# Kernel optimization log

Measured on AMD Instinct MI355X. Metric: run time of the kernel, lower is better.

## Reference

```python
import jax, jax.numpy as jnp
import numpy as np

VOXEL_SIZE = (0.075, 0.075, 0.2)
PC_MIN = (-54.0, -54.0, -5.0)
GRID = (1440, 1440, 40)      # (gx, gy, gz) = round((pc_max - pc_min) / voxel_size)
MAX_PTS = 10                 # max points per voxel
MAX_VOX = 160000             # max voxels (train)


def setup_inputs() -> dict:
    key = jax.random.key(0)
    N, C = 2_000_000, 5
    u = jax.random.uniform(key, (N, C), dtype=jnp.float32)
    lo = jnp.array([-54.0, -54.0, -5.0, 0.0, 0.0], jnp.float32)
    span = jnp.array([108.0, 108.0, 8.0, 1.0, 1.0], jnp.float32)
    return {"points": u * span + lo}


def reference(points):
    # Faithful PointToVoxel semantics: bin points into voxels, voxels ordered by
    # first point occurrence (hash-table insertion order), cap points-per-voxel
    # and voxel count, return (voxels, coords_zyx, num_points_per_voxel).
    N, C = points.shape
    gx, gy, gz = GRID
    vsize = jnp.array(VOXEL_SIZE, jnp.float32)
    pmin = jnp.array(PC_MIN, jnp.float32)

    c = jnp.floor((points[:, :3] - pmin) / vsize).astype(jnp.int32)  # [N,3] xyz voxel coords
    valid = jnp.all((c >= 0) & (c < jnp.array([gx, gy, gz], jnp.int32)), axis=1)
    lin = (c[:, 2].astype(jnp.int64) * gy + c[:, 1]) * gx + c[:, 0]  # z-major linear id
    sent = jnp.int64(gx) * gy * gz                                    # sentinel for invalid
    lin = jnp.where(valid, lin, sent)

    # Sort by (voxel id, point index): groups points by voxel, earliest point first.
    order = jnp.argsort(lin * N + jnp.arange(N, dtype=jnp.int64))
    slin = lin[order]
    valid_s = slin < sent
    new = jnp.concatenate([valid_s[:1], (slin[1:] != slin[:-1]) & valid_s[1:]])
    gid = jnp.maximum(jnp.cumsum(new.astype(jnp.int32)) - 1, 0)       # group id per sorted point

    # First (smallest) original point index per voxel group -> insertion order rank.
    first_idx = jnp.full((N,), N, jnp.int32).at[gid].min(
        jnp.where(valid_s, order, N).astype(jnp.int32), mode="drop")
    ranks = jnp.argsort(jnp.argsort(first_idx)).astype(jnp.int32)     # voxel insertion rank

    # Slot of each point within its voxel group.
    idx32 = jnp.arange(N, dtype=jnp.int32)
    starts = jax.lax.associative_scan(jnp.maximum, jnp.where(new, idx32, 0))
    pos = idx32 - starts

    r = ranks[gid]
    keep = valid_s & (r < MAX_VOX) & (pos < MAX_PTS)
    vox_idx = jnp.where(keep, r, MAX_VOX)   # MAX_VOX = out-of-bounds -> dropped
    slot = jnp.where(keep, pos, 0)

    voxels = jnp.zeros((MAX_VOX, MAX_PTS, C), points.dtype).at[vox_idx, slot].set(
        points[order], mode="drop")
    num_points = jnp.zeros((MAX_VOX,), jnp.int32).at[vox_idx].add(1, mode="drop")
    czyx = c[:, ::-1][order]                # spconv returns coords as (z, y, x)
    coords = jnp.zeros((MAX_VOX, 3), jnp.int32).at[vox_idx].set(czyx, mode="drop")
    return voxels, coords, num_points
```

## Files before the change

### kernel.cpp

```cpp
#include <hip/hip_runtime.h>

#define GX 1440
#define GY 1440
#define GZ 40
#define MAX_PTS 10
#define MAX_VOX 160000
#define NC 40
#define CAPC 65536
#define CHUNK 4096
#define L2CHUNKS (CAPC / CHUNK)
#define NFINE 10240
#define CAPB2 512
#define PA_BLOCKS 1024
#define PA_ITERS 8
#define GSTRIDE 16
#define EMPTY32 0xFFFFFFFFu
#define EMPTY64 0xFFFFFFFFFFFFFFFFull
#define BCAP (1 << 19)
#define NBLKB (BCAP / 256)
#define TAILB ((MAX_VOX + 255) / 256)
#define HG 65536
#define MCAP 12
#define ST_PARTIAL (1ull << 62)
#define ST_PREFIX  (2ull << 62)
#define ST_VAL     ((1ull << 62) - 1)

__global__ void pa1_scatter(const float* __restrict__ pts, int n,
                            unsigned long long* __restrict__ pairs1,
                            int* __restrict__ gcur1) {
    __shared__ int hist[NC];
    if (threadIdx.x < NC) hist[threadIdx.x] = 0;
    __syncthreads();
    int per = (n + PA_BLOCKS - 1) / PA_BLOCKS;
    int i0 = blockIdx.x * per;
    int i1 = i0 + per; if (i1 > n) i1 = n;
    int lin[PA_ITERS];
#pragma unroll
    for (int u = 0; u < PA_ITERS; ++u) {
        int i = i0 + u * 256 + (int)threadIdx.x;
        int l = -1;
        if (i < i1) {
            float x = pts[i * 5 + 0];
            float y = pts[i * 5 + 1];
            float z = pts[i * 5 + 2];
            int cx = (int)floorf((x - (-54.0f)) / 0.075f);
            int cy = (int)floorf((y - (-54.0f)) / 0.075f);
            int cz = (int)floorf((z - (-5.0f)) / 0.2f);
            if (cx >= 0 && cx < GX && cy >= 0 && cy < GY && cz >= 0 && cz < GZ)
                l = (cz * GY + cy) * GX + cx;
        }
        lin[u] = l;
        if (l >= 0) atomicAdd(&hist[l >> 21], 1);
    }
    __syncthreads();
    if (threadIdx.x < NC) {
        int h = hist[threadIdx.x];
        hist[threadIdx.x] =
            (h > 0) ? atomicAdd(&gcur1[threadIdx.x * GSTRIDE], h) : 0;
    }
    __syncthreads();
#pragma unroll
    for (int u = 0; u < PA_ITERS; ++u) {
        int l = lin[u];
        if (l < 0) continue;
        int i = i0 + u * 256 + (int)threadIdx.x;
        int c = l >> 21;
        int pos = atomicAdd(&hist[c], 1);
        if (pos < CAPC)
            pairs1[(size_t)c * CAPC + pos] =
                ((unsigned long long)(unsigned)l << 32) | (unsigned)i;
    }
}

__global__ void pa2_scatter(const unsigned long long* __restrict__ pairs1,
                            const int* __restrict__ gcur1,
                            unsigned long long* __restrict__ pairs2,
                            int* __restrict__ gcur2) {
    __shared__ int cur[256];
    int c = blockIdx.x >> 4;
    int j = blockIdx.x & (L2CHUNKS - 1);
    cur[threadIdx.x] = 0;
    __syncthreads();
    int cnt = gcur1[c * GSTRIDE]; if (cnt > CAPC) cnt = CAPC;
    int t0 = j * CHUNK;
    int t1 = t0 + CHUNK; if (t1 > cnt) t1 = cnt;
    const unsigned long long* bp = pairs1 + (size_t)c * CAPC;
    unsigned long long pr[CHUNK / 256];
#pragma unroll
    for (int u = 0; u < CHUNK / 256; ++u) {
        int t = t0 + u * 256 + (int)threadIdx.x;
        pr[u] = (t < t1) ? bp[t] : EMPTY64;
        if (pr[u] != EMPTY64)
            atomicAdd(&cur[(unsigned)(pr[u] >> 45) & 255u], 1);
    }
    __syncthreads();
    {
        int h = cur[threadIdx.x];
        cur[threadIdx.x] =
            (h > 0)
                ? atomicAdd(&gcur2[((c << 8) + threadIdx.x) * GSTRIDE], h)
                : 0;
    }
    __syncthreads();
#pragma unroll
    for (int u = 0; u < CHUNK / 256; ++u) {
        if (pr[u] == EMPTY64) continue;
        int f = (int)((unsigned)(pr[u] >> 45) & 255u);
        int pos = atomicAdd(&cur[f], 1);
        if (pos < CAPB2)
            pairs2[(size_t)((c << 8) + f) * CAPB2 + pos] = pr[u];
    }
}

__global__ void pb_build(const unsigned long long* __restrict__ pairs2,
                         const int* __restrict__ gcur2,
                         unsigned char* __restrict__ marks8,
                         unsigned int* __restrict__ hkey,
                         unsigned int* __restrict__ hcnt,
                         unsigned int* __restrict__ hmem) {
    __shared__ unsigned int mn[8192];
    __shared__ unsigned int multibit[256];
    int fid = blockIdx.x;
    int n = gcur2[fid * GSTRIDE]; if (n > CAPB2) n = CAPB2;
    uint4* mn4 = (uint4*)mn;
    uint4 e4 = make_uint4(EMPTY32, EMPTY32, EMPTY32, EMPTY32);
#pragma unroll
    for (int u = 0; u < 8; ++u) mn4[u * 256 + threadIdx.x] = e4;
    multibit[threadIdx.x] = 0;
    __syncthreads();
    const unsigned long long* bp = pairs2 + (size_t)fid * CAPB2;
    unsigned int lcell[CAPB2 / 256];
    unsigned int lidx[CAPB2 / 256];
#pragma unroll
    for (int u = 0; u < CAPB2 / 256; ++u) {
        int t = u * 256 + (int)threadIdx.x;
        unsigned cell = EMPTY32, idx = 0;
        if (t < n) {
            unsigned long long pr = bp[t];
            cell = ((unsigned)(pr >> 32)) & 8191u;
            idx = (unsigned)pr;
        }
        lcell[u] = cell;
        lidx[u] = idx;
        if (cell != EMPTY32) atomicMin(&mn[cell], idx);
    }
    __syncthreads();
#pragma unroll
    for (int u = 0; u < CAPB2 / 256; ++u) {
        unsigned cell = lcell[u];
        if (cell == EMPTY32) continue;
        unsigned m = mn[cell];
        if (m != lidx[u]) {
            atomicOr(&multibit[cell >> 5], 1u << (cell & 31));
            if (m < BCAP) {
                unsigned key = m + 1u;
                unsigned h = (m * 2654435761u) >> 16;
                while (true) {
                    unsigned prev = atomicCAS(&hkey[h], 0u, key);
                    if (prev == 0u || prev == key) break;
                    h = (h + 1) & (HG - 1);
                }
                unsigned pos = atomicAdd(&hcnt[h], 1u);
                if (pos < MCAP) hmem[h * MCAP + pos] = lidx[u];
            }
        }
    }
    __syncthreads();
#pragma unroll
    for (int u = 0; u < CAPB2 / 256; ++u) {
        unsigned cell = lcell[u];
        if (cell != EMPTY32 && mn[cell] == lidx[u] && lidx[u] < BCAP)
            marks8[lidx[u]] = (unsigned char)(
                1u + ((multibit[cell >> 5] >> (cell & 31)) & 1u));
    }
}

__global__ void pfx_fill(const float* __restrict__ pts,
                         const unsigned char* __restrict__ marks8,
                         unsigned long long* __restrict__ dstate,
                         const unsigned int* __restrict__ hkey,
                         const unsigned int* __restrict__ hcnt,
                         const unsigned int* __restrict__ hmem,
                         float* __restrict__ vox, float* __restrict__ coords,
                         float* __restrict__ nump) {
    int t = blockIdx.x;
    int tid = threadIdx.x, lane = tid & 63, wv = tid >> 6;
    if (t >= NBLKB) {
        int r = (t - NBLKB) * 256 + tid;
        if (r >= MAX_VOX) return;
        unsigned long long s = 0;
        if (lane == 0)
            do { s = atomicAdd(&dstate[NBLKB - 1], 0ull); } while ((s >> 62) != 2);
        int V = (int)__shfl((int)(s & ST_VAL), 0, 64);
        if (V > MAX_VOX) V = MAX_VOX;
        if (r < V) return;
        float* row = vox + (size_t)r * (MAX_PTS * 5);
        for (int k = 0; k < MAX_PTS * 5; ++k) row[k] = 0.0f;
        coords[r * 3 + 0] = 0.0f;
        coords[r * 3 + 1] = 0.0f;
        coords[r * 3 + 2] = 0.0f;
        nump[r] = 0.0f;
        return;
    }
    __shared__ unsigned cw[4];
    __shared__ int sh_prefix;
    int i = t * 256 + tid;
    int m8 = marks8[i];
    unsigned long long b = __ballot(m8 != 0);
    if (lane == 0) cw[wv] = (unsigned)__popcll(b);
    __syncthreads();
    int c = (int)(cw[0] + cw[1] + cw[2] + cw[3]);
    if (tid == 0) atomicExch(&dstate[t], ST_PARTIAL | (unsigned long long)c);
    if (wv == 0) {
        int agg = 0;
        int base = t;
        bool done = (t == 0);
        while (!done) {
            int j = base - 1 - lane;
            unsigned long long s;
            do {
                s = (j >= 0) ? atomicAdd(&dstate[j], 0ull) : ST_PREFIX;
            } while ((s >> 62) == 0);
            unsigned long long pm = __ballot((s >> 62) == 2);
            int val = (int)(s & ST_VAL);
            if (pm) {
                int k = (int)(__ffsll((long long)pm) - 1);
                int contrib = (lane <= k) ? val : 0;
                for (int o = 32; o >= 1; o >>= 1) contrib += __shfl_down(contrib, o, 64);
                agg += __shfl(contrib, 0, 64);
                done = true;
            } else {
                int contrib = val;
                for (int o = 32; o >= 1; o >>= 1) contrib += __shfl_down(contrib, o, 64);
                agg += __shfl(contrib, 0, 64);
                base -= 64;
            }
        }
        if (lane == 0) {
            sh_prefix = agg;
            atomicExch(&dstate[t], ST_PREFIX | (unsigned long long)(agg + c));
        }
    }
    __syncthreads();
    if (!m8) return;
    int off0 = 0;
    for (int w = 0; w < wv; ++w) off0 += (int)cw[w];
    int r = sh_prefix + off0 + (int)__popcll(b & ((1ull << lane) - 1ull));
    if (r >= MAX_VOX) return;
    float p5[5];
#pragma unroll
    for (int j = 0; j < 5; ++j) p5[j] = pts[(size_t)i * 5 + j];
    int cx = (int)floorf((p5[0] - (-54.0f)) / 0.075f);
    int cy = (int)floorf((p5[1] - (-54.0f)) / 0.075f);
    int cz = (int)floorf((p5[2] - (-5.0f)) / 0.2f);
    coords[r * 3 + 0] = (float)cz;
    coords[r * 3 + 1] = (float)cy;
    coords[r * 3 + 2] = (float)cx;
    float* row = vox + (size_t)r * (MAX_PTS * 5);
    if (m8 == 1) {
        nump[r] = 1.0f;
#pragma unroll
        for (int j = 0; j < 5; ++j) row[j] = p5[j];
        for (int k = 5; k < MAX_PTS * 5; ++k) row[k] = 0.0f;
    } else {
        unsigned key = (unsigned)i + 1u;
        unsigned h = ((unsigned)i * 2654435761u) >> 16;
        while (hkey[h] != key) h = (h + 1) & (HG - 1);
        int cc = (int)hcnt[h];
        int cnt = 1 + cc;
        int np = cnt < MAX_PTS ? cnt : MAX_PTS;
        nump[r] = (float)np;
        int km = cc < MCAP ? cc : MCAP;
        int sel[MCAP];
        for (int j = 0; j < km; ++j) sel[j] = (int)hmem[h * MCAP + j];
        for (int a = 1; a < km; ++a) {
            int v = sel[a], p = a;
            while (p > 0 && sel[p - 1] > v) { sel[p] = sel[p - 1]; --p; }
            sel[p] = v;
        }
#pragma unroll
        for (int j = 0; j < 5; ++j) row[j] = p5[j];
        for (int s = 1; s < MAX_PTS; ++s) {
            if (s < np) {
                const float* q5 = pts + (size_t)sel[s - 1] * 5;
#pragma unroll
                for (int j = 0; j < 5; ++j) row[s * 5 + j] = q5[j];
            } else {
#pragma unroll
                for (int j = 0; j < 5; ++j) row[s * 5 + j] = 0.0f;
            }
        }
    }
}

extern "C" void kernel_launch(void* const* d_in, const int* in_sizes, int n_in,
                              void* d_out, int out_size, void* d_ws, size_t ws_size,
                              hipStream_t stream) {
    const float* pts = (const float*)d_in[0];
    int n = in_sizes[0] / 5;

    unsigned long long* pairs1 = (unsigned long long*)d_ws;
    unsigned long long* pairs2 = pairs1 + (size_t)NC * CAPC;
    unsigned int* hmem = (unsigned int*)(pairs2 + (size_t)NFINE * CAPB2);
    int* gcur1 = (int*)(hmem + (size_t)HG * MCAP);
    int* gcur2 = gcur1 + NC * GSTRIDE;
    unsigned int* hcnt = (unsigned int*)(gcur2 + NFINE * GSTRIDE);
    unsigned long long* dstate = (unsigned long long*)(hcnt + HG);
    unsigned int* hkey = (unsigned int*)(dstate + NBLKB);
    unsigned char* marks8 = (unsigned char*)(hkey + HG);

    size_t zbytes = (size_t)(NC + NFINE) * GSTRIDE * 4 + (size_t)HG * 4 +
                    (size_t)NBLKB * 8 + (size_t)HG * 4 + BCAP;
    hipMemsetAsync(gcur1, 0, zbytes, stream);

    float* out = (float*)d_out;
    float* vox = out;
    float* coords = out + (size_t)MAX_VOX * MAX_PTS * 5;
    float* nump = coords + (size_t)MAX_VOX * 3;

    pa1_scatter<<<PA_BLOCKS, 256, 0, stream>>>(pts, n, pairs1, gcur1);
    pa2_scatter<<<NC * L2CHUNKS, 256, 0, stream>>>(pairs1, gcur1, pairs2, gcur2);
    pb_build<<<NFINE, 256, 0, stream>>>(pairs2, gcur2, marks8, hkey, hcnt, hmem);
    pfx_fill<<<NBLKB + TAILB, 256, 0, stream>>>(pts, marks8, dstate, hkey, hcnt,
                                                hmem, vox, coords, nump);
}
```

Measured before the change: 178.0 us.

## Replace global member hash with bucket rescan and stage output rows in LDS

```diff
diff --git a/kernel.cpp b/kernel.cpp
--- a/kernel.cpp
+++ b/kernel.cpp
@@ -19,8 +19,6 @@
 #define BCAP (1 << 19)
 #define NBLKB (BCAP / 256)
 #define TAILB ((MAX_VOX + 255) / 256)
-#define HG 65536
-#define MCAP 12
 #define ST_PARTIAL (1ull << 62)
 #define ST_PREFIX  (2ull << 62)
 #define ST_VAL     ((1ull << 62) - 1)
@@ -114,10 +112,7 @@
 
 __global__ void pb_build(const unsigned long long* __restrict__ pairs2,
                          const int* __restrict__ gcur2,
-                         unsigned char* __restrict__ marks8,
-                         unsigned int* __restrict__ hkey,
-                         unsigned int* __restrict__ hcnt,
-                         unsigned int* __restrict__ hmem) {
+                         unsigned char* __restrict__ marks8) {
     __shared__ unsigned int mn[8192];
     __shared__ unsigned int multibit[256];
     int fid = blockIdx.x;
@@ -148,22 +143,8 @@
 #pragma unroll
     for (int u = 0; u < CAPB2 / 256; ++u) {
         unsigned cell = lcell[u];
-        if (cell == EMPTY32) continue;
-        unsigned m = mn[cell];
-        if (m != lidx[u]) {
+        if (cell != EMPTY32 && mn[cell] != lidx[u])
             atomicOr(&multibit[cell >> 5], 1u << (cell & 31));
-            if (m < BCAP) {
-                unsigned key = m + 1u;
-                unsigned h = (m * 2654435761u) >> 16;
-                while (true) {
-                    unsigned prev = atomicCAS(&hkey[h], 0u, key);
-                    if (prev == 0u || prev == key) break;
-                    h = (h + 1) & (HG - 1);
-                }
-                unsigned pos = atomicAdd(&hcnt[h], 1u);
-                if (pos < MCAP) hmem[h * MCAP + pos] = lidx[u];
-            }
-        }
     }
     __syncthreads();
 #pragma unroll
@@ -178,9 +159,8 @@
 __global__ void pfx_fill(const float* __restrict__ pts,
                          const unsigned char* __restrict__ marks8,
                          unsigned long long* __restrict__ dstate,
-                         const unsigned int* __restrict__ hkey,
-                         const unsigned int* __restrict__ hcnt,
-                         const unsigned int* __restrict__ hmem,
+                         const unsigned long long* __restrict__ pairs2,
+                         const int* __restrict__ gcur2,
                          float* __restrict__ vox, float* __restrict__ coords,
                          float* __restrict__ nump) {
     int t = blockIdx.x;
@@ -204,6 +184,9 @@
     }
     __shared__ unsigned cw[4];
     __shared__ int sh_prefix;
+    __shared__ float srow[256 * 51];
+    __shared__ float scrd[256 * 3];
+    __shared__ float snum[256];
     int i = t * 256 + tid;
     int m8 = marks8[i];
     unsigned long long b = __ballot(m8 != 0);
@@ -242,55 +225,82 @@
         }
     }
     __syncthreads();
-    if (!m8) return;
-    int off0 = 0;
-    for (int w = 0; w < wv; ++w) off0 += (int)cw[w];
-    int r = sh_prefix + off0 + (int)__popcll(b & ((1ull << lane) - 1ull));
-    if (r >= MAX_VOX) return;
-    float p5[5];
-#pragma unroll
-    for (int j = 0; j < 5; ++j) p5[j] = pts[(size_t)i * 5 + j];
-    int cx = (int)floorf((p5[0] - (-54.0f)) / 0.075f);
-    int cy = (int)floorf((p5[1] - (-54.0f)) / 0.075f);
-    int cz = (int)floorf((p5[2] - (-5.0f)) / 0.2f);
-    coords[r * 3 + 0] = (float)cz;
-    coords[r * 3 + 1] = (float)cy;
-    coords[r * 3 + 2] = (float)cx;
-    float* row = vox + (size_t)r * (MAX_PTS * 5);
-    if (m8 == 1) {
-        nump[r] = 1.0f;
-#pragma unroll
-        for (int j = 0; j < 5; ++j) row[j] = p5[j];
-        for (int k = 5; k < MAX_PTS * 5; ++k) row[k] = 0.0f;
-    } else {
-        unsigned key = (unsigned)i + 1u;
-        unsigned h = ((unsigned)i * 2654435761u) >> 16;
-        while (hkey[h] != key) h = (h + 1) & (HG - 1);
-        int cc = (int)hcnt[h];
-        int cnt = 1 + cc;
-        int np = cnt < MAX_PTS ? cnt : MAX_PTS;
-        nump[r] = (float)np;
-        int km = cc < MCAP ? cc : MCAP;
-        int sel[MCAP];
-        for (int j = 0; j < km; ++j) sel[j] = (int)hmem[h * MCAP + j];
-        for (int a = 1; a < km; ++a) {
-            int v = sel[a], p = a;
-            while (p > 0 && sel[p - 1] > v) { sel[p] = sel[p - 1]; --p; }
-            sel[p] = v;
-        }
-#pragma unroll
-        for (int j = 0; j < 5; ++j) row[j] = p5[j];
-        for (int s = 1; s < MAX_PTS; ++s) {
-            if (s < np) {
-                const float* q5 = pts + (size_t)sel[s - 1] * 5;
-#pragma unroll
-                for (int j = 0; j < 5; ++j) row[s * 5 + j] = q5[j];
+    int base = sh_prefix;
+    if (m8) {
+        int off0 = 0;
+        for (int w = 0; w < wv; ++w) off0 += (int)cw[w];
+        int lr = off0 + (int)__popcll(b & ((1ull << lane) - 1ull));
+        if (base + lr < MAX_VOX) {
+            float p5[5];
+#pragma unroll
+            for (int j = 0; j < 5; ++j) p5[j] = pts[(size_t)i * 5 + j];
+            int cx = (int)floorf((p5[0] - (-54.0f)) / 0.075f);
+            int cy = (int)floorf((p5[1] - (-54.0f)) / 0.075f);
+            int cz = (int)floorf((p5[2] - (-5.0f)) / 0.2f);
+            scrd[lr * 3 + 0] = (float)cz;
+            scrd[lr * 3 + 1] = (float)cy;
+            scrd[lr * 3 + 2] = (float)cx;
+            float* row = &srow[lr * 51];
+            if (m8 == 1) {
+                snum[lr] = 1.0f;
+#pragma unroll
+                for (int j = 0; j < 5; ++j) row[j] = p5[j];
+                for (int k = 5; k < MAX_PTS * 5; ++k) row[k] = 0.0f;
             } else {
-#pragma unroll
-                for (int j = 0; j < 5; ++j) row[s * 5 + j] = 0.0f;
+                int lin = (cz * GY + cy) * GX + cx;
+                int fid = lin >> 13;
+                unsigned cell = (unsigned)lin & 8191u;
+                int n2 = gcur2[fid * GSTRIDE]; if (n2 > CAPB2) n2 = CAPB2;
+                const unsigned long long* bp = pairs2 + (size_t)fid * CAPB2;
+                int sel[MAX_PTS];
+                int cnt = 0, totc = 0;
+                for (int tt = 0; tt < n2; ++tt) {
+                    unsigned long long pr = bp[tt];
+                    if ((((unsigned)(pr >> 32)) & 8191u) == cell) {
+                        int idx = (int)(unsigned)pr;
+                        ++totc;
+                        if (cnt < MAX_PTS) {
+                            int p = cnt++;
+                            while (p > 0 && sel[p - 1] > idx) { sel[p] = sel[p - 1]; --p; }
+                            sel[p] = idx;
+                        } else if (idx < sel[MAX_PTS - 1]) {
+                            int p = MAX_PTS - 1;
+                            while (p > 0 && sel[p - 1] > idx) { sel[p] = sel[p - 1]; --p; }
+                            sel[p] = idx;
+                        }
+                    }
+                }
+                int np = totc < MAX_PTS ? totc : MAX_PTS;
+                snum[lr] = (float)np;
+                for (int s = 0; s < MAX_PTS; ++s) {
+                    if (s < np) {
+                        const float* q5 = pts + (size_t)sel[s] * 5;
+#pragma unroll
+                        for (int j = 0; j < 5; ++j) row[s * 5 + j] = q5[j];
+                    } else {
+#pragma unroll
+                        for (int j = 0; j < 5; ++j) row[s * 5 + j] = 0.0f;
+                    }
+                }
             }
         }
     }
+    __syncthreads();
+    int rows = c;
+    if (base >= MAX_VOX) rows = 0;
+    else if (base + rows > MAX_VOX) rows = MAX_VOX - base;
+    if (rows == 0) return;
+    float* dvox = vox + (size_t)base * (MAX_PTS * 5);
+    int tot = rows * 50;
+    for (int k = tid; k < tot; k += 256) {
+        int rr = k / 50;
+        dvox[k] = srow[rr * 51 + (k - rr * 50)];
+    }
+    int tot3 = rows * 3;
+    float* dcrd = coords + (size_t)base * 3;
+    for (int k = tid; k < tot3; k += 256) dcrd[k] = scrd[k];
+    float* dnum = nump + base;
+    for (int k = tid; k < rows; k += 256) dnum[k] = snum[k];
 }
 
 extern "C" void kernel_launch(void* const* d_in, const int* in_sizes, int n_in,
@@ -301,16 +311,13 @@
 
     unsigned long long* pairs1 = (unsigned long long*)d_ws;
     unsigned long long* pairs2 = pairs1 + (size_t)NC * CAPC;
-    unsigned int* hmem = (unsigned int*)(pairs2 + (size_t)NFINE * CAPB2);
-    int* gcur1 = (int*)(hmem + (size_t)HG * MCAP);
+    int* gcur1 = (int*)(pairs2 + (size_t)NFINE * CAPB2);
     int* gcur2 = gcur1 + NC * GSTRIDE;
-    unsigned int* hcnt = (unsigned int*)(gcur2 + NFINE * GSTRIDE);
-    unsigned long long* dstate = (unsigned long long*)(hcnt + HG);
-    unsigned int* hkey = (unsigned int*)(dstate + NBLKB);
-    unsigned char* marks8 = (unsigned char*)(hkey + HG);
-
-    size_t zbytes = (size_t)(NC + NFINE) * GSTRIDE * 4 + (size_t)HG * 4 +
-                    (size_t)NBLKB * 8 + (size_t)HG * 4 + BCAP;
+    unsigned long long* dstate = (unsigned long long*)(gcur2 + NFINE * GSTRIDE);
+    unsigned char* marks8 = (unsigned char*)(dstate + NBLKB);
+
+    size_t zbytes = (size_t)(NC + NFINE) * GSTRIDE * 4 +
+                    (size_t)NBLKB * 8 + BCAP;
     hipMemsetAsync(gcur1, 0, zbytes, stream);
 
     float* out = (float*)d_out;
@@ -320,7 +327,7 @@
 
     pa1_scatter<<<PA_BLOCKS, 256, 0, stream>>>(pts, n, pairs1, gcur1);
     pa2_scatter<<<NC * L2CHUNKS, 256, 0, stream>>>(pairs1, gcur1, pairs2, gcur2);
-    pb_build<<<NFINE, 256, 0, stream>>>(pairs2, gcur2, marks8, hkey, hcnt, hmem);
-    pfx_fill<<<NBLKB + TAILB, 256, 0, stream>>>(pts, marks8, dstate, hkey, hcnt,
-                                                hmem, vox, coords, nump);
-}
+    pb_build<<<NFINE, 256, 0, stream>>>(pairs2, gcur2, marks8);
+    pfx_fill<<<NBLKB + TAILB, 256, 0, stream>>>(pts, marks8, dstate, pairs2,
+                                                gcur2, vox, coords, nump);
+}
```

Result: slower. 236.0 us (+32.6%).
